# Optimization experiments

Hardware: AMD Instinct MI355X
Metric: run time of the kernel (lower is better)

The kernel has to match this reference:

```python
import jax, jax.numpy as jnp
import numpy as np
from jax import lax

B, L, D_MODEL = 2, 1024, 1024
EXPAND, D_STATE, D_CONV = 2, 16, 4
D_INNER = EXPAND * D_MODEL
DT_RANK = D_MODEL // 16  # ceil(1024/16) = 64
D_FF = 4 * D_MODEL


def setup_inputs() -> dict:
    key = jax.random.key(0)
    ks = jax.random.split(key, 20)
    s = lambda *sh: 1.0 / np.sqrt(sh[-1])
    inp = {
        "x": jax.random.normal(ks[0], (B, L, D_MODEL), jnp.float32),
        "ln1_w": jnp.ones((D_MODEL,), jnp.float32),
        "ln1_b": jnp.zeros((D_MODEL,), jnp.float32),
        "W_in": jax.random.normal(ks[1], (2 * D_INNER, D_MODEL), jnp.float32) * s(D_MODEL),
        "conv_w": jax.random.normal(ks[2], (D_INNER, D_CONV), jnp.float32) * s(D_CONV),
        "conv_b": jnp.zeros((D_INNER,), jnp.float32),
        "W_xproj": jax.random.normal(ks[3], (DT_RANK + 2 * D_STATE, D_INNER), jnp.float32) * s(D_INNER),
        "W_dt": jax.random.normal(ks[4], (D_INNER, DT_RANK), jnp.float32) * s(DT_RANK),
        "b_dt": jax.random.uniform(ks[5], (D_INNER,), jnp.float32, -4.0, -2.0),  # dt bias ~ small softplus
        "A_log": jnp.log(jnp.broadcast_to(jnp.arange(1, D_STATE + 1, dtype=jnp.float32), (D_INNER, D_STATE))),
        "D": jnp.ones((D_INNER,), jnp.float32),
        "W_out": jax.random.normal(ks[6], (D_MODEL, D_INNER), jnp.float32) * s(D_INNER),
        "ln2_w": jnp.ones((D_MODEL,), jnp.float32),
        "ln2_b": jnp.zeros((D_MODEL,), jnp.float32),
        "W1": jax.random.normal(ks[7], (D_FF, D_MODEL), jnp.float32) * s(D_MODEL),
        "b1": jnp.zeros((D_FF,), jnp.float32),
        "W2": jax.random.normal(ks[8], (D_MODEL, D_FF), jnp.float32) * s(D_FF),
        "b2": jnp.zeros((D_MODEL,), jnp.float32),
    }
    return inp


def _layernorm(x, w, b, eps=1e-5):
    mu = jnp.mean(x, axis=-1, keepdims=True)
    var = jnp.var(x, axis=-1, keepdims=True)
    return (x - mu) * lax.rsqrt(var + eps) * w + b


def _mamba(h, W_in, conv_w, conv_b, W_xproj, W_dt, b_dt, A_log, D, W_out):
    # in_proj -> [B, L, 2*d_inner]
    xz = jnp.einsum("bld,ed->ble", h, W_in)
    u, z = xz[..., :D_INNER], xz[..., D_INNER:]
    # causal depthwise conv over time
    uc = jnp.transpose(u, (0, 2, 1))  # [B, d_inner, L]
    uc = lax.conv_general_dilated(
        uc, conv_w[:, None, :], window_strides=(1,), padding=[(D_CONV - 1, 0)],
        dimension_numbers=("NCH", "OIH", "NCH"), feature_group_count=D_INNER)
    uc = jax.nn.silu(uc + conv_b[None, :, None])
    u = jnp.transpose(uc, (0, 2, 1))  # [B, L, d_inner]
    # input-dependent dt, B, C
    x_db = jnp.einsum("bld,ed->ble", u, W_xproj)
    dt = jax.nn.softplus(jnp.einsum("blr,dr->bld", x_db[..., :DT_RANK], W_dt) + b_dt)
    Bm = x_db[..., DT_RANK:DT_RANK + D_STATE]  # [B, L, d_state]
    Cm = x_db[..., DT_RANK + D_STATE:]         # [B, L, d_state]
    A = -jnp.exp(A_log)                        # [d_inner, d_state]

    def step(hst, t):
        dt_t, B_t, C_t, u_t = t  # [B,d_inner], [B,ds], [B,ds], [B,d_inner]
        dA = jnp.exp(dt_t[:, :, None] * A)                       # [B,d_inner,d_state]
        hst = dA * hst + dt_t[:, :, None] * B_t[:, None, :] * u_t[:, :, None]
        y_t = jnp.einsum("bds,bs->bd", hst, C_t)
        return hst, y_t

    h0 = jnp.zeros((u.shape[0], D_INNER, D_STATE), u.dtype)
    xs = (jnp.swapaxes(dt, 0, 1), jnp.swapaxes(Bm, 0, 1), jnp.swapaxes(Cm, 0, 1), jnp.swapaxes(u, 0, 1))
    _, ys = lax.scan(step, h0, xs)
    y = jnp.swapaxes(ys, 0, 1) + u * D  # skip term D*u
    y = y * jax.nn.silu(z)
    return jnp.einsum("ble,de->bld", y, W_out)


def reference(x, ln1_w, ln1_b, W_in, conv_w, conv_b, W_xproj, W_dt, b_dt, A_log, D,
              W_out, ln2_w, ln2_b, W1, b1, W2, b2):
    x = x + _mamba(_layernorm(x, ln1_w, ln1_b), W_in, conv_w, conv_b, W_xproj, W_dt, b_dt, A_log, D, W_out)
    h = _layernorm(x, ln2_w, ln2_b)
    ffn = jnp.einsum("blf,df->bld", jax.nn.relu(jnp.einsum("bld,fd->blf", h, W1) + b1), W2) + b2
    return x + ffn
```

## Files before the change

kernel.cpp:

```cpp
#include <hip/hip_runtime.h>

typedef unsigned short u16;
typedef unsigned int   u32;
typedef short   bf16x8 __attribute__((ext_vector_type(8)));
typedef float   f32x4  __attribute__((ext_vector_type(4)));
typedef u16     u16x4  __attribute__((ext_vector_type(4)));

__device__ __forceinline__ u16 f2b(float f) {
    u32 u = __builtin_bit_cast(u32, f);
    u32 r = u + 0x7FFFu + ((u >> 16) & 1u);
    return (u16)(r >> 16);
}
__device__ __forceinline__ float b2f(u16 h) {
    u32 u = ((u32)h) << 16;
    return __builtin_bit_cast(float, u);
}
__device__ __forceinline__ u16x4 f4_to_b4(float4 v) {
    u16x4 o; o.x = f2b(v.x); o.y = f2b(v.y); o.z = f2b(v.z); o.w = f2b(v.w);
    return o;
}

__device__ __forceinline__ float fexp2(float x) {
    float r;
    asm("v_exp_f32 %0, %1" : "=v"(r) : "v"(x));
    return r;
}
__device__ __forceinline__ float flog2(float x) {
    float r;
    asm("v_log_f32 %0, %1" : "=v"(r) : "v"(x));
    return r;
}

template <int CTRL>
__device__ __forceinline__ float dpp_add(float p) {
    int pi = __builtin_bit_cast(int, p);
    int q  = __builtin_amdgcn_update_dpp(pi, pi, CTRL, 0xF, 0xF, false);
    return p + __builtin_bit_cast(float, q);
}
#define DPP_XOR1 0xB1
#define DPP_XOR2 0x4E
#define DPP_HMIR 0x141
#define DPP_MIR  0x140

#define MROWS   2048
#define NSEG    16
#define SEGT    64
#define L2E     1.44269504088896340736f
#define LN2     0.69314718055994530942f

#define GLDS(g, l) __builtin_amdgcn_global_load_lds(                      \
    (const __attribute__((address_space(1))) void*)(g),                   \
    (__attribute__((address_space(3))) void*)(l), 16, 0, 0)

__global__ __launch_bounds__(256) void cvt_all(const float* __restrict__ W_in,
                                               const float* __restrict__ W_out,
                                               const float* __restrict__ W1,
                                               const float* __restrict__ W2,
                                               const float* __restrict__ W_dt,
                                               u16* __restrict__ Winb,
                                               u16* __restrict__ Woutb,
                                               u16* __restrict__ W1b,
                                               u16* __restrict__ W2b,
                                               u16* __restrict__ Wdtb) {
    const int i = blockIdx.x * 256 + threadIdx.x;
    const float* src; u16* dst; int off;
    if (i < 1048576)      { src = W_in;  dst = Winb;  off = i; }
    else if (i < 1572864) { src = W_out; dst = Woutb; off = i - 1048576; }
    else if (i < 2621440) { src = W1;    dst = W1b;   off = i - 1572864; }
    else if (i < 3670016) { src = W2;    dst = W2b;   off = i - 2621440; }
    else                  { src = W_dt;  dst = Wdtb;  off = i - 3670016; }
    float4 v = ((const float4*)src)[off];
    ((u16x4*)dst)[off] = f4_to_b4(v);
}

__global__ __launch_bounds__(256) void pad_xproj_kernel(const float* __restrict__ in,
                                                        u16* __restrict__ out) {
    int i = blockIdx.x * 256 + threadIdx.x;
    int r = i >> 9, c4 = i & 511;
    float4 v = make_float4(0.f, 0.f, 0.f, 0.f);
    if (r < 96) v = ((const float4*)(in + (size_t)r * 2048))[c4];
    ((u16x4*)(out + (size_t)r * 2048))[c4] = f4_to_b4(v);
}

__global__ __launch_bounds__(256) void ln_kernel(const float* __restrict__ x,
                                                 const float* __restrict__ w,
                                                 const float* __restrict__ b,
                                                 u16* __restrict__ out) {
    const int row = blockIdx.x;
    const int tid = threadIdx.x;
    const float4 v = ((const float4*)(x + (size_t)row * 1024))[tid];
    float s = v.x + v.y + v.z + v.w;
    float q = v.x * v.x + v.y * v.y + v.z * v.z + v.w * v.w;
#pragma unroll
    for (int off = 1; off < 64; off <<= 1) {
        s += __shfl_xor(s, off, 64);
        q += __shfl_xor(q, off, 64);
    }
    __shared__ float ss[4], qq[4];
    const int wave = tid >> 6;
    if ((tid & 63) == 0) { ss[wave] = s; qq[wave] = q; }
    __syncthreads();
    s = ss[0] + ss[1] + ss[2] + ss[3];
    q = qq[0] + qq[1] + qq[2] + qq[3];
    const float mean = s * (1.f / 1024.f);
    const float var  = q * (1.f / 1024.f) - mean * mean;
    const float rstd = rsqrtf(var + 1e-5f);
    const float4 wv = ((const float4*)w)[tid];
    const float4 bv = ((const float4*)b)[tid];
    float4 o;
    o.x = (v.x - mean) * rstd * wv.x + bv.x;
    o.y = (v.y - mean) * rstd * wv.y + bv.y;
    o.z = (v.z - mean) * rstd * wv.z + bv.z;
    o.w = (v.w - mean) * rstd * wv.w + bv.w;
    ((u16x4*)(out + (size_t)row * 1024))[tid] = f4_to_b4(o);
}

__global__ __launch_bounds__(256) void conv_kernel(const u16* __restrict__ xzu,
                                                   const float* __restrict__ cw,
                                                   const float* __restrict__ cb,
                                                   u16* __restrict__ utl) {
    const int idx = blockIdx.x * 256 + threadIdx.x;
    const int row = idx >> 9;
    const int d4  = idx & 511;
    const int d   = d4 * 4;
    const int bb  = row >> 10;
    const int t   = row & 1023;
    float w0[4], w1[4], w2[4], w3[4];
    *(float4*)w0 = ((const float4*)cw)[d + 0];
    *(float4*)w1 = ((const float4*)cw)[d + 1];
    *(float4*)w2 = ((const float4*)cw)[d + 2];
    *(float4*)w3 = ((const float4*)cw)[d + 3];
    float4 a = ((const float4*)cb)[d4];
#pragma unroll
    for (int j = 0; j < 4; ++j) {
        const int tt = t - 3 + j;
        if (tt >= 0) {
            const u16x4 uv = *(const u16x4*)(xzu + ((size_t)(bb * 1024 + tt)) * 2048 + d);
            a.x += b2f(uv.x) * w0[j];
            a.y += b2f(uv.y) * w1[j];
            a.z += b2f(uv.z) * w2[j];
            a.w += b2f(uv.w) * w3[j];
        }
    }
    float4 o;
    o.x = a.x / (1.f + __expf(-a.x));
    o.y = a.y / (1.f + __expf(-a.y));
    o.z = a.z / (1.f + __expf(-a.z));
    o.w = a.w / (1.f + __expf(-a.w));
    *(u16x4*)(utl + (((size_t)(d >> 4)) * 2048 + row) * 16 + (d & 15)) = f4_to_b4(o);
}

template <int EPI>
__global__ __launch_bounds__(512) void gemm_tb(const u16* __restrict__ A,
                                               const u16* __restrict__ Bw,
                                               void* __restrict__ Cptr,
                                               void* __restrict__ Cptr2,
                                               const float* __restrict__ bias,
                                               int M, int N, int K, int KS) {
    const int nbm = gridDim.x, nbn = gridDim.y;
    const int nwg = nbm * nbn;
    const int id  = blockIdx.x + nbm * blockIdx.y;
    const int sw  = (nwg >= 8) ? ((id & 7) * (nwg >> 3) + (id >> 3)) : id;
    const int bm  = sw % nbm, bn = sw / nbm;

    __shared__ u16 Asm[4][128 * 32];
    __shared__ u16 Bsm[4][128 * 32];
    const int tid  = threadIdx.x;
    const int kz   = blockIdx.z;
    const int lane = tid & 63;
    const int wave = tid >> 6;
    const int wm   = wave >> 1, wn = wave & 1;
    const u16* Ag = A  + (size_t)bm * 128 * K;
    const u16* Bg = Bw + (size_t)bn * 128 * K;
    const int r0 = tid >> 2;
    const int sg = (tid & 3) * 8;
    const int k0 = kz * KS;
    const int nk = KS >> 5;
    const int fr = lane & 15, fk = (lane >> 4) * 8;

#define STG(bf, kk)                                                            \
    {                                                                          \
        const int kof = k0 + (kk) * 32;                                        \
        GLDS(Ag + (size_t)r0 * K + kof + sg, &Asm[bf][tid * 8]);               \
        GLDS(Bg + (size_t)r0 * K + kof + sg, &Bsm[bf][tid * 8]);               \
    }

    f32x4 acc[2][4] = {};
    STG(0, 0); STG(1, 1); STG(2, 2);
    int buf = 0;
    for (int k = 0; k < nk; ++k) {
        if (k < nk - 2)       asm volatile("s_waitcnt vmcnt(4)" ::: "memory");
        else if (k == nk - 2) asm volatile("s_waitcnt vmcnt(2)" ::: "memory");
        else                  asm volatile("s_waitcnt vmcnt(0)" ::: "memory");
        __builtin_amdgcn_s_barrier();
        bf16x8 a[2], b[4];
#pragma unroll
        for (int m = 0; m < 2; ++m)
            a[m] = *(const bf16x8*)&Asm[buf][(wm * 32 + m * 16 + fr) * 32 + fk];
#pragma unroll
        for (int n = 0; n < 4; ++n)
            b[n] = *(const bf16x8*)&Bsm[buf][(wn * 64 + n * 16 + fr) * 32 + fk];
        if (k + 3 < nk) STG((buf + 3) & 3, k + 3);
#pragma unroll
        for (int m = 0; m < 2; ++m)
#pragma unroll
            for (int n = 0; n < 4; ++n)
                acc[m][n] = __builtin_amdgcn_mfma_f32_16x16x32_bf16(a[m], b[n], acc[m][n], 0, 0, 0);
        buf = (buf + 1) & 3;
    }
#undef STG

    const int fq = lane >> 4;
#pragma unroll
    for (int m = 0; m < 2; ++m) {
#pragma unroll
        for (int n = 0; n < 4; ++n) {
            const int row0 = bm * 128 + wm * 32 + m * 16 + fq * 4;
            const int col  = bn * 128 + wn * 64 + n * 16 + fr;
#pragma unroll
            for (int j = 0; j < 4; ++j) {
                float v = acc[m][n][j];
                if constexpr (EPI == 3) {
                    v += bias[col];
                    ((u16*)Cptr)[(size_t)(row0 + j) * N + col] = f2b(fmaxf(v, 0.f));
                } else if constexpr (EPI == 5) {
                    if (col < 2048) {
                        ((u16*)Cptr)[(size_t)(row0 + j) * 2048 + col] = f2b(v);
                    } else {
                        const float sv = v / (1.f + __expf(-v));
                        const int zc = col - 2048;
                        ((u16*)Cptr2)[(((size_t)(zc >> 4)) * 2048 + row0 + j) * 16 + (zc & 15)]
                            = f2b(sv);
                    }
                } else {
                    ((float*)Cptr)[(size_t)kz * M * N + (size_t)(row0 + j) * N + col] = v;
                }
            }
        }
    }
}

__global__ __launch_bounds__(256) void gemm_xp(const u16* __restrict__ utl,
                                               const u16* __restrict__ Bw,
                                               float* __restrict__ part) {
    const int nwg = 16;
    const int id  = blockIdx.x;
    const int sw  = (id & 7) * (nwg >> 3) + (id >> 3);
    const int bm  = sw;
    __shared__ u16 Asm[4][128 * 32];
    __shared__ u16 Bsm[4][128 * 32];
    const int tid  = threadIdx.x;
    const int kz   = blockIdx.z;
    const int lane = tid & 63;
    const int wave = tid >> 6;
    const int wm   = wave >> 1, wn = wave & 1;
    const u16* Bg = Bw;
    const int r0 = tid >> 2;
    const int pc = tid & 3;
    const int sg = pc * 8;
    const int k0 = kz * 256;
    const int fr = lane & 15, fk = (lane >> 4) * 8;

#define STGX(bf, kk)                                                                     \
    {                                                                                    \
        const int kof = k0 + (kk) * 32;                                                  \
        const int kc  = kof >> 4;                                                        \
        GLDS(utl + ((size_t)(kc + (pc >> 1)) * 2048 + bm * 128 + r0) * 16 + (pc & 1) * 8,\
             &Asm[bf][tid * 8]);                                                         \
        GLDS(utl + ((size_t)(kc + (pc >> 1)) * 2048 + bm * 128 + r0 + 64) * 16 + (pc & 1) * 8,\
             &Asm[bf][(tid + 256) * 8]);                                                 \
        GLDS(Bg + (size_t)r0 * 2048 + kof + sg, &Bsm[bf][tid * 8]);                      \
        GLDS(Bg + (size_t)(r0 + 64) * 2048 + kof + sg, &Bsm[bf][(tid + 256) * 8]);       \
    }

    f32x4 acc[4][4] = {};
    STGX(0, 0); STGX(1, 1); STGX(2, 2);
    int buf = 0;
    const int nk = 8;
    for (int k = 0; k < nk; ++k) {
        if (k < nk - 2)       asm volatile("s_waitcnt vmcnt(8)" ::: "memory");
        else if (k == nk - 2) asm volatile("s_waitcnt vmcnt(4)" ::: "memory");
        else                  asm volatile("s_waitcnt vmcnt(0)" ::: "memory");
        __builtin_amdgcn_s_barrier();
        bf16x8 a[4], b[4];
#pragma unroll
        for (int m = 0; m < 4; ++m)
            a[m] = *(const bf16x8*)&Asm[buf][(wm * 64 + m * 16 + fr) * 32 + fk];
#pragma unroll
        for (int n = 0; n < 4; ++n)
            b[n] = *(const bf16x8*)&Bsm[buf][(wn * 64 + n * 16 + fr) * 32 + fk];
        if (k + 3 < nk) STGX((buf + 3) & 3, k + 3);
#pragma unroll
        for (int m = 0; m < 4; ++m)
#pragma unroll
            for (int n = 0; n < 4; ++n)
                acc[m][n] = __builtin_amdgcn_mfma_f32_16x16x32_bf16(a[m], b[n], acc[m][n], 0, 0, 0);
        buf = (buf + 1) & 3;
    }
#undef STGX

    const int fq = lane >> 4;
    float* Cp = part + (size_t)kz * MROWS * 128;
#pragma unroll
    for (int m = 0; m < 4; ++m) {
#pragma unroll
        for (int n = 0; n < 4; ++n) {
            const int row0 = bm * 128 + wm * 64 + m * 16 + fq * 4;
            const int col  = wn * 64 + n * 16 + fr;
#pragma unroll
            for (int j = 0; j < 4; ++j)
                Cp[(size_t)(row0 + j) * 128 + col] = acc[m][n][j];
        }
    }
}

__global__ __launch_bounds__(256) void xproj_combine(const float* __restrict__ part,
                                                     u16* __restrict__ xdbr,
                                                     float* __restrict__ bcp) {
    int i = blockIdx.x * 256 + threadIdx.x;
    int row = i >> 5, c4 = i & 31;
    if (c4 >= 24) return;
    float4 s = make_float4(0.f, 0.f, 0.f, 0.f);
#pragma unroll
    for (int p = 0; p < 8; ++p) {
        float4 v = ((const float4*)(part + (size_t)p * MROWS * 128 + (size_t)row * 128))[c4];
        s.x += v.x; s.y += v.y; s.z += v.z; s.w += v.w;
    }
    if (c4 < 16) {
        ((u16x4*)(xdbr + (size_t)row * 64))[c4] = f4_to_b4(s);
    } else {
        const int e0 = (c4 - 16) * 4;
        float sv[4] = {s.x, s.y, s.z, s.w};
#pragma unroll
        for (int j = 0; j < 4; ++j) {
            const int e = e0 + j;
            const int st  = (e < 16) ? e : (e - 16);
            const int isc = (e < 16) ? 0 : 1;
            bcp[(size_t)(row >> 1) * 64 + st * 4 + (row & 1) * 2 + isc] = sv[j];
        }
    }
}

__device__ __forceinline__ void compute_dtu_tile(const u16* __restrict__ xdbr,
                                                 const u16* __restrict__ Wdtb,
                                                 const float* __restrict__ b_dt,
                                                 const u16* __restrict__ utile,
                                                 float* __restrict__ du_s,
                                                 size_t t0, int d0, int w, int l) {
    const int fr = l & 15, fk = (l >> 4) * 8;
    const bf16x8 a0 = *(const bf16x8*)(xdbr + (t0 + w * 16 + fr) * 64 + fk);
    const bf16x8 a1 = *(const bf16x8*)(xdbr + (t0 + w * 16 + fr) * 64 + 32 + fk);
    const bf16x8 b0 = *(const bf16x8*)(Wdtb + (size_t)(d0 + fr) * 64 + fk);
    const bf16x8 b1 = *(const bf16x8*)(Wdtb + (size_t)(d0 + fr) * 64 + 32 + fk);
    const float bdt = b_dt[d0 + fr];
    f32x4 acc = {};
    acc = __builtin_amdgcn_mfma_f32_16x16x32_bf16(a0, b0, acc, 0, 0, 0);
    acc = __builtin_amdgcn_mfma_f32_16x16x32_bf16(a1, b1, acc, 0, 0, 0);
#pragma unroll
    for (int j = 0; j < 4; ++j) {
        const int row = w * 16 + (l >> 4) * 4 + j;
        float v = acc[j] + bdt;
        const float sp = flog2(1.f + fexp2(v * L2E)) * LN2;
        v = (v > 20.f) ? v : sp;
        const float uval = b2f(utile[(t0 + row) * 16 + fr]);
        float2 dv; dv.x = v; dv.y = v * uval;
        *(float2*)&du_s[(row >> 1) * 66 + fr * 4 + (row & 1) * 2] = dv;
    }
}

__device__ __forceinline__ void stage_bc(const float* __restrict__ bcp,
                                         float* __restrict__ bc_s,
                                         size_t p0, int w, int l) {
    const int pr = (w << 3) + (l >> 4);
    const int pc = (l & 15) << 2;
    GLDS(bcp + (p0 + pr) * 64 + pc,     &bc_s[(w << 9)]);
    GLDS(bcp + (p0 + pr + 4) * 64 + pc, &bc_s[(w << 9) + 256]);
}

__global__ __launch_bounds__(256) void scan_pass1(const u16* __restrict__ xdbr,
                                                  const u16* __restrict__ Wdtb,
                                                  const float* __restrict__ b_dt,
                                                  const u16* __restrict__ utl,
                                                  const float* __restrict__ bcp,
                                                  const float* __restrict__ A_log,
                                                  float* __restrict__ Qarr,
                                                  float* __restrict__ Sarr) {
    __shared__ __align__(16) float du_s[32 * 66];
    __shared__ __align__(16) float bc_s[32 * 64];

    const int tid = threadIdx.x;
    const int l   = tid & 63;
    const int w   = tid >> 6;
    const int s   = l & 15;
    const int g   = (w << 2) | (l >> 4);
    const int d0  = blockIdx.x << 4;
    const int b   = blockIdx.y;
    const int seg = blockIdx.z;
    const int d   = d0 + g;
    const size_t t0 = (size_t)b * 1024 + (size_t)seg * SEGT;
    const u16* utile = utl + (size_t)(d0 >> 4) * 2048 * 16;

    stage_bc(bcp, bc_s, t0 >> 1, w, l);
    compute_dtu_tile(xdbr, Wdtb, b_dt, utile, du_s, t0, d0, w, l);

    const float As2 = -__expf(A_log[d * 16 + s]) * L2E;
    asm volatile("s_waitcnt vmcnt(0) lgkmcnt(0)" ::: "memory");
    __builtin_amdgcn_s_barrier();

    float Q = 0.f, S = 0.f;
#pragma unroll 8
    for (int t2 = 0; t2 < 32; ++t2) {
        const float4 du4 = *(const float4*)&du_s[t2 * 66 + g * 4];
        const float4 BC2 = *(const float4*)&bc_s[t2 * 64 + s * 4];
        S += du4.x;
        Q = fexp2(du4.x * As2) * Q + du4.y * BC2.x;
        S += du4.z;
        Q = fexp2(du4.z * As2) * Q + du4.w * BC2.z;
    }
    Qarr[(((size_t)seg * 2 + b) * 2048 + d) * 16 + s] = Q;
    if (s == 0) Sarr[((size_t)seg * 2 + b) * 2048 + d] = S;
}

__global__ __launch_bounds__(256) void scan_prefix(const float* __restrict__ Qarr,
                                                   const float* __restrict__ Sarr,
                                                   const float* __restrict__ A_log,
                                                   float* __restrict__ H0) {
    const int tid = threadIdx.x;
    const int d   = (blockIdx.x << 4) + (tid >> 4);
    const int s   = tid & 15;
    const int b   = blockIdx.y;
    const float As2 = -__expf(A_log[d * 16 + s]) * L2E;
    float h = 0.f;
#pragma unroll
    for (int i = 0; i < NSEG; ++i) {
        const size_t base = ((size_t)i * 2 + b) * 2048 + d;
        H0[base * 16 + s] = h;
        h = fexp2(As2 * Sarr[base]) * h + Qarr[base * 16 + s];
    }
}

__global__ __launch_bounds__(256) void scan_pass2(const u16* __restrict__ xdbr,
                                                  const u16* __restrict__ Wdtb,
                                                  const float* __restrict__ b_dt,
                                                  const u16* __restrict__ utl,
                                                  const float* __restrict__ bcp,
                                                  const u16* __restrict__ zst,
                                                  const float* __restrict__ A_log,
                                                  const float* __restrict__ Dp,
                                                  const float* __restrict__ H0,
                                                  u16* __restrict__ ymul) {
    __shared__ __align__(16) float du_s[32 * 66];
    __shared__ __align__(16) float bc_s[32 * 64];

    const int tid = threadIdx.x;
    const int l   = tid & 63;
    const int w   = tid >> 6;
    const int s   = l & 15;
    const int g   = (w << 2) | (l >> 4);
    const int d0  = blockIdx.x << 4;
    const int b   = blockIdx.y;
    const int seg = blockIdx.z;
    const int d   = d0 + g;
    const size_t t0 = (size_t)b * 1024 + (size_t)seg * SEGT;
    const u16* utile = utl + (size_t)(d0 >> 4) * 2048 * 16;
    const u16* ztile = zst + (size_t)(d0 >> 4) * 2048 * 16;

    stage_bc(bcp, bc_s, t0 >> 1, w, l);
    compute_dtu_tile(xdbr, Wdtb, b_dt, utile, du_s, t0, d0, w, l);

    const float As2 = -__expf(A_log[d * 16 + s]) * L2E;
    float h = H0[(((size_t)seg * 2 + b) * 2048 + d) * 16 + s];

    asm volatile("s_waitcnt vmcnt(0) lgkmcnt(0)" ::: "memory");
    __builtin_amdgcn_s_barrier();

    float pk[4];
#pragma unroll
    for (int c = 0; c < 4; ++c) {
        pk[c] = 0.f;
#pragma unroll
        for (int q = 0; q < 8; ++q) {
            const int t2 = c * 8 + q;
            const float4 du4 = *(const float4*)&du_s[t2 * 66 + g * 4];
            const float4 BC2 = *(const float4*)&bc_s[t2 * 64 + s * 4];
            h = fexp2(du4.x * As2) * h + du4.y * BC2.x;
            float p = h * BC2.y;
            p = dpp_add<DPP_XOR1>(p);
            p = dpp_add<DPP_XOR2>(p);
            p = dpp_add<DPP_HMIR>(p);
            p = dpp_add<DPP_MIR>(p);
            {
                const unsigned long long km = 0x0001000100010001ULL << (2 * q);
                asm("v_cndmask_b32 %0, %0, %1, %2" : "+v"(pk[c]) : "v"(p), "s"(km));
            }
            h = fexp2(du4.z * As2) * h + du4.w * BC2.z;
            p = h * BC2.w;
            p = dpp_add<DPP_XOR1>(p);
            p = dpp_add<DPP_XOR2>(p);
            p = dpp_add<DPP_HMIR>(p);
            p = dpp_add<DPP_MIR>(p);
            {
                const unsigned long long km = 0x0001000100010001ULL << (2 * q + 1);
                asm("v_cndmask_b32 %0, %0, %1, %2" : "+v"(pk[c]) : "v"(p), "s"(km));
            }
        }
    }

    __builtin_amdgcn_s_barrier();
    float* p_s = du_s;
#pragma unroll
    for (int c = 0; c < 4; ++c) {
        const int row = c * 16 + s;
        p_s[row * 16 + (g ^ (row & 12))] = pk[c];
    }

    asm volatile("s_waitcnt lgkmcnt(0)" ::: "memory");
    __builtin_amdgcn_s_barrier();

    {
        const int tt = tid >> 2, cc = (tid & 3) << 2;
        const float4 pv = *(const float4*)&p_s[tt * 16 + (cc ^ (tt & 12))];
        const u16x4  uv = *(const u16x4*)(utile + (t0 + tt) * 16 + cc);
        const u16x4  zs = *(const u16x4*)(ztile + (t0 + tt) * 16 + cc);
        const float4 Dv = *(const float4*)(Dp + d0 + cc);
        float4 o;
        o.x = (pv.x + b2f(uv.x) * Dv.x) * b2f(zs.x);
        o.y = (pv.y + b2f(uv.y) * Dv.y) * b2f(zs.y);
        o.z = (pv.z + b2f(uv.z) * Dv.z) * b2f(zs.z);
        o.w = (pv.w + b2f(uv.w) * Dv.w) * b2f(zs.w);
        *(u16x4*)(ymul + (t0 + tt) * 2048 + d0 + cc) = f4_to_b4(o);
    }
}

__global__ __launch_bounds__(256) void ffn2_combine(const float* __restrict__ part,
                                                    const float* __restrict__ x2,
                                                    const float* __restrict__ b2,
                                                    float* __restrict__ out) {
    int i = blockIdx.x * 256 + threadIdx.x;
    float4 s = ((const float4*)x2)[i];
    float4 bv = ((const float4*)b2)[i & 255];
    s.x += bv.x; s.y += bv.y; s.z += bv.z; s.w += bv.w;
#pragma unroll
    for (int p = 0; p < 4; ++p) {
        float4 v = ((const float4*)(part + (size_t)p * MROWS * 1024))[i];
        s.x += v.x; s.y += v.y; s.z += v.z; s.w += v.w;
    }
    ((float4*)out)[i] = s;
}

__global__ __launch_bounds__(256) void outproj_combine_ln2(const float* __restrict__ x,
                                                           const float* __restrict__ part,
                                                           const float* __restrict__ w,
                                                           const float* __restrict__ b,
                                                           float* __restrict__ x2,
                                                           u16* __restrict__ h2) {
    const int row = blockIdx.x;
    const int tid = threadIdx.x;
    float4 v = ((const float4*)(x + (size_t)row * 1024))[tid];
    float4 p0 = ((const float4*)(part + (size_t)row * 1024))[tid];
    float4 p1 = ((const float4*)(part + (size_t)MROWS * 1024 + (size_t)row * 1024))[tid];
    v.x += p0.x + p1.x; v.y += p0.y + p1.y; v.z += p0.z + p1.z; v.w += p0.w + p1.w;
    ((float4*)(x2 + (size_t)row * 1024))[tid] = v;
    float s = v.x + v.y + v.z + v.w;
    float q = v.x * v.x + v.y * v.y + v.z * v.z + v.w * v.w;
#pragma unroll
    for (int off = 1; off < 64; off <<= 1) {
        s += __shfl_xor(s, off, 64);
        q += __shfl_xor(q, off, 64);
    }
    __shared__ float ss[4], qq[4];
    const int wave = tid >> 6;
    if ((tid & 63) == 0) { ss[wave] = s; qq[wave] = q; }
    __syncthreads();
    s = ss[0] + ss[1] + ss[2] + ss[3];
    q = qq[0] + qq[1] + qq[2] + qq[3];
    const float mean = s * (1.f / 1024.f);
    const float var  = q * (1.f / 1024.f) - mean * mean;
    const float rstd = rsqrtf(var + 1e-5f);
    const float4 wv = ((const float4*)w)[tid];
    const float4 bv = ((const float4*)b)[tid];
    float4 o;
    o.x = (v.x - mean) * rstd * wv.x + bv.x;
    o.y = (v.y - mean) * rstd * wv.y + bv.y;
    o.z = (v.z - mean) * rstd * wv.z + bv.z;
    o.w = (v.w - mean) * rstd * wv.w + bv.w;
    ((u16x4*)(h2 + (size_t)row * 1024))[tid] = f4_to_b4(o);
}

extern "C" void kernel_launch(void* const* d_in, const int* in_sizes, int n_in,
                              void* d_out, int out_size, void* d_ws, size_t ws_size,
                              hipStream_t stream) {
    const float* x      = (const float*)d_in[0];
    const float* ln1_w  = (const float*)d_in[1];
    const float* ln1_b  = (const float*)d_in[2];
    const float* W_in   = (const float*)d_in[3];
    const float* conv_w = (const float*)d_in[4];
    const float* conv_b = (const float*)d_in[5];
    const float* W_xproj= (const float*)d_in[6];
    const float* W_dt   = (const float*)d_in[7];
    const float* b_dt   = (const float*)d_in[8];
    const float* A_log  = (const float*)d_in[9];
    const float* Dvec   = (const float*)d_in[10];
    const float* W_out  = (const float*)d_in[11];
    const float* ln2_w  = (const float*)d_in[12];
    const float* ln2_b  = (const float*)d_in[13];
    const float* W1     = (const float*)d_in[14];
    const float* b1     = (const float*)d_in[15];
    const float* W2     = (const float*)d_in[16];
    const float* b2     = (const float*)d_in[17];
    float* out = (float*)d_out;
    char*  ws  = (char*)d_ws;
    const size_t MB = 1024ull * 1024ull;

    u16*   h1b   = (u16*)(ws + 0);
    u16*   xzu   = (u16*)(ws + 4 * MB);
    u16*   zst   = (u16*)(ws + 12 * MB);
    u16*   utl   = (u16*)(ws + 20 * MB);
    float* parts = (float*)(ws + 28 * MB);
    float* bcp   = (float*)(ws + 36 * MB);
    u16*   xdbr  = (u16*)(ws + 36 * MB + 256 * 1024);
    u16*   Wdtb  = (u16*)(ws + 36 * MB + 512 * 1024);
    u16*   ymul  = (u16*)(ws + 37 * MB);
    float* Qarr  = (float*)(ws + 45 * MB);
    float* Sarr  = (float*)(ws + 49 * MB);
    float* H0    = (float*)(ws + 50 * MB);
    float* x2    = (float*)(ws + 54 * MB);
    u16*   Winb  = (u16*)(ws + 62 * MB);
    u16*   Woutb = (u16*)(ws + 70 * MB);
    u16*   W1b   = (u16*)(ws + 74 * MB);
    u16*   W2b   = (u16*)(ws + 82 * MB);
    u16*   Wxpb  = (u16*)(ws + 90 * MB);
    u16*   h2b   = h1b;
    float* opart = (float*)(ws + 4 * MB);
    u16*   f1    = (u16*)(ws + 4 * MB);
    float* fpart = (float*)(ws + 20 * MB);

    cvt_all<<<14464, 256, 0, stream>>>(W_in, W_out, W1, W2, W_dt,
                                       Winb, Woutb, W1b, W2b, Wdtb);
    pad_xproj_kernel<<<256, 256, 0, stream>>>(W_xproj, Wxpb);

    ln_kernel<<<2048, 256, 0, stream>>>(x, ln1_w, ln1_b, h1b);
    gemm_tb<5><<<dim3(16, 32, 1), 512, 0, stream>>>(h1b, Winb, xzu, zst, nullptr,
                                                    MROWS, 4096, 1024, 1024);
    conv_kernel<<<4096, 256, 0, stream>>>(xzu, conv_w, conv_b, utl);
    gemm_xp<<<dim3(16, 1, 8), 256, 0, stream>>>(utl, Wxpb, parts);
    xproj_combine<<<256, 256, 0, stream>>>(parts, xdbr, bcp);
    scan_pass1<<<dim3(128, 2, NSEG), 256, 0, stream>>>(xdbr, Wdtb, b_dt, utl, bcp, A_log,
                                                       Qarr, Sarr);
    scan_prefix<<<dim3(128, 2), 256, 0, stream>>>(Qarr, Sarr, A_log, H0);
    scan_pass2<<<dim3(128, 2, NSEG), 256, 0, stream>>>(xdbr, Wdtb, b_dt, utl, bcp, zst,
                                                       A_log, Dvec, H0, ymul);
    gemm_tb<10><<<dim3(16, 8, 2), 512, 0, stream>>>(ymul, Woutb, opart, nullptr, nullptr,
                                                    MROWS, 1024, 2048, 1024);
    outproj_combine_ln2<<<2048, 256, 0, stream>>>(x, opart, ln2_w, ln2_b, x2, h2b);
    gemm_tb<3><<<dim3(16, 32, 1), 512, 0, stream>>>(h2b, W1b, f1, nullptr, b1,
                                                    MROWS, 4096, 1024, 1024);
    gemm_tb<10><<<dim3(16, 8, 4), 512, 0, stream>>>(f1, W2b, fpart, nullptr, nullptr,
                                                    MROWS, 1024, 4096, 1024);
    ffn2_combine<<<2048, 256, 0, stream>>>(fpart, x2, b2, out);
}
```

Before: 217.0 us.

## Shrink GEMM LDS ring to three stages and pack B-only buffer for scan pass1

Both GEMM kernels move from a 4-slot, 3-ahead shared-memory prefetch ring to a 3-slot, 2-ahead ring, with adjusted vmcnt waits. This cuts LDS use per block, which can raise occupancy, at the cost of less latency hiding. Separately, xproj_combine now also writes a packed B-only array so scan_pass1 can stage half as much data into LDS with a single direct global-to-LDS load, instead of staging the interleaved B/C buffer.

```diff
diff --git a/kernel.cpp b/kernel.cpp
--- a/kernel.cpp
+++ b/kernel.cpp
@@ -163,8 +163,8 @@
     const int sw  = (nwg >= 8) ? ((id & 7) * (nwg >> 3) + (id >> 3)) : id;
     const int bm  = sw % nbm, bn = sw / nbm;
 
-    __shared__ u16 Asm[4][128 * 32];
-    __shared__ u16 Bsm[4][128 * 32];
+    __shared__ u16 Asm[3][128 * 32];
+    __shared__ u16 Bsm[3][128 * 32];
     const int tid  = threadIdx.x;
     const int kz   = blockIdx.z;
     const int lane = tid & 63;
@@ -186,12 +186,11 @@
     }
 
     f32x4 acc[2][4] = {};
-    STG(0, 0); STG(1, 1); STG(2, 2);
+    STG(0, 0); STG(1, 1);
     int buf = 0;
     for (int k = 0; k < nk; ++k) {
-        if (k < nk - 2)       asm volatile("s_waitcnt vmcnt(4)" ::: "memory");
-        else if (k == nk - 2) asm volatile("s_waitcnt vmcnt(2)" ::: "memory");
-        else                  asm volatile("s_waitcnt vmcnt(0)" ::: "memory");
+        if (k < nk - 1) asm volatile("s_waitcnt vmcnt(2)" ::: "memory");
+        else            asm volatile("s_waitcnt vmcnt(0)" ::: "memory");
         __builtin_amdgcn_s_barrier();
         bf16x8 a[2], b[4];
 #pragma unroll
@@ -200,13 +199,16 @@
 #pragma unroll
         for (int n = 0; n < 4; ++n)
             b[n] = *(const bf16x8*)&Bsm[buf][(wn * 64 + n * 16 + fr) * 32 + fk];
-        if (k + 3 < nk) STG((buf + 3) & 3, k + 3);
+        if (k + 2 < nk) {
+            const int slot = (buf + 2) % 3;
+            STG(slot, k + 2);
+        }
 #pragma unroll
         for (int m = 0; m < 2; ++m)
 #pragma unroll
             for (int n = 0; n < 4; ++n)
                 acc[m][n] = __builtin_amdgcn_mfma_f32_16x16x32_bf16(a[m], b[n], acc[m][n], 0, 0, 0);
-        buf = (buf + 1) & 3;
+        buf = (buf == 2) ? 0 : buf + 1;
     }
 #undef STG
 
@@ -247,8 +249,8 @@
     const int id  = blockIdx.x;
     const int sw  = (id & 7) * (nwg >> 3) + (id >> 3);
     const int bm  = sw;
-    __shared__ u16 Asm[4][128 * 32];
-    __shared__ u16 Bsm[4][128 * 32];
+    __shared__ u16 Asm[3][128 * 32];
+    __shared__ u16 Bsm[3][128 * 32];
     const int tid  = threadIdx.x;
     const int kz   = blockIdx.z;
     const int lane = tid & 63;
@@ -274,13 +276,12 @@
     }
 
     f32x4 acc[4][4] = {};
-    STGX(0, 0); STGX(1, 1); STGX(2, 2);
+    STGX(0, 0); STGX(1, 1);
     int buf = 0;
     const int nk = 8;
     for (int k = 0; k < nk; ++k) {
-        if (k < nk - 2)       asm volatile("s_waitcnt vmcnt(8)" ::: "memory");
-        else if (k == nk - 2) asm volatile("s_waitcnt vmcnt(4)" ::: "memory");
-        else                  asm volatile("s_waitcnt vmcnt(0)" ::: "memory");
+        if (k < nk - 1) asm volatile("s_waitcnt vmcnt(4)" ::: "memory");
+        else            asm volatile("s_waitcnt vmcnt(0)" ::: "memory");
         __builtin_amdgcn_s_barrier();
         bf16x8 a[4], b[4];
 #pragma unroll
@@ -289,13 +290,16 @@
 #pragma unroll
         for (int n = 0; n < 4; ++n)
             b[n] = *(const bf16x8*)&Bsm[buf][(wn * 64 + n * 16 + fr) * 32 + fk];
-        if (k + 3 < nk) STGX((buf + 3) & 3, k + 3);
+        if (k + 2 < nk) {
+            const int slot = (buf + 2) % 3;
+            STGX(slot, k + 2);
+        }
 #pragma unroll
         for (int m = 0; m < 4; ++m)
 #pragma unroll
             for (int n = 0; n < 4; ++n)
                 acc[m][n] = __builtin_amdgcn_mfma_f32_16x16x32_bf16(a[m], b[n], acc[m][n], 0, 0, 0);
-        buf = (buf + 1) & 3;
+        buf = (buf == 2) ? 0 : buf + 1;
     }
 #undef STGX
 
@@ -316,7 +320,8 @@
 
 __global__ __launch_bounds__(256) void xproj_combine(const float* __restrict__ part,
                                                      u16* __restrict__ xdbr,
-                                                     float* __restrict__ bcp) {
+                                                     float* __restrict__ bcp,
+                                                     float* __restrict__ bpk) {
     int i = blockIdx.x * 256 + threadIdx.x;
     int row = i >> 5, c4 = i & 31;
     if (c4 >= 24) return;
@@ -337,6 +342,8 @@
             const int st  = (e < 16) ? e : (e - 16);
             const int isc = (e < 16) ? 0 : 1;
             bcp[(size_t)(row >> 1) * 64 + st * 4 + (row & 1) * 2 + isc] = sv[j];
+            if (e < 16)
+                bpk[(size_t)(row >> 1) * 32 + st * 2 + (row & 1)] = sv[j];
         }
     }
 }
@@ -381,12 +388,12 @@
                                                   const u16* __restrict__ Wdtb,
                                                   const float* __restrict__ b_dt,
                                                   const u16* __restrict__ utl,
-                                                  const float* __restrict__ bcp,
+                                                  const float* __restrict__ bpk,
                                                   const float* __restrict__ A_log,
                                                   float* __restrict__ Qarr,
                                                   float* __restrict__ Sarr) {
     __shared__ __align__(16) float du_s[32 * 66];
-    __shared__ __align__(16) float bc_s[32 * 64];
+    __shared__ __align__(16) float bp_s[32 * 32];
 
     const int tid = threadIdx.x;
     const int l   = tid & 63;
@@ -400,7 +407,7 @@
     const size_t t0 = (size_t)b * 1024 + (size_t)seg * SEGT;
     const u16* utile = utl + (size_t)(d0 >> 4) * 2048 * 16;
 
-    stage_bc(bcp, bc_s, t0 >> 1, w, l);
+    GLDS(bpk + ((t0 >> 1) + (tid >> 3)) * 32 + ((tid & 7) << 2), &bp_s[w << 8]);
     compute_dtu_tile(xdbr, Wdtb, b_dt, utile, du_s, t0, d0, w, l);
 
     const float As2 = -__expf(A_log[d * 16 + s]) * L2E;
@@ -411,11 +418,11 @@
 #pragma unroll 8
     for (int t2 = 0; t2 < 32; ++t2) {
         const float4 du4 = *(const float4*)&du_s[t2 * 66 + g * 4];
-        const float4 BC2 = *(const float4*)&bc_s[t2 * 64 + s * 4];
+        const float2 Bp  = *(const float2*)&bp_s[t2 * 32 + s * 2];
         S += du4.x;
-        Q = fexp2(du4.x * As2) * Q + du4.y * BC2.x;
+        Q = fexp2(du4.x * As2) * Q + du4.y * Bp.x;
         S += du4.z;
-        Q = fexp2(du4.z * As2) * Q + du4.w * BC2.z;
+        Q = fexp2(du4.z * As2) * Q + du4.w * Bp.y;
     }
     Qarr[(((size_t)seg * 2 + b) * 2048 + d) * 16 + s] = Q;
     if (s == 0) Sarr[((size_t)seg * 2 + b) * 2048 + d] = S;
@@ -620,6 +627,7 @@
     float* bcp   = (float*)(ws + 36 * MB);
     u16*   xdbr  = (u16*)(ws + 36 * MB + 256 * 1024);
     u16*   Wdtb  = (u16*)(ws + 36 * MB + 512 * 1024);
+    float* bpk   = (float*)(ws + 36 * MB + 768 * 1024);
     u16*   ymul  = (u16*)(ws + 37 * MB);
     float* Qarr  = (float*)(ws + 45 * MB);
     float* Sarr  = (float*)(ws + 49 * MB);
@@ -644,8 +652,8 @@
                                                     MROWS, 4096, 1024, 1024);
     conv_kernel<<<4096, 256, 0, stream>>>(xzu, conv_w, conv_b, utl);
     gemm_xp<<<dim3(16, 1, 8), 256, 0, stream>>>(utl, Wxpb, parts);
-    xproj_combine<<<256, 256, 0, stream>>>(parts, xdbr, bcp);
-    scan_pass1<<<dim3(128, 2, NSEG), 256, 0, stream>>>(xdbr, Wdtb, b_dt, utl, bcp, A_log,
+    xproj_combine<<<256, 256, 0, stream>>>(parts, xdbr, bcp, bpk);
+    scan_pass1<<<dim3(128, 2, NSEG), 256, 0, stream>>>(xdbr, Wdtb, b_dt, utl, bpk, A_log,
                                                        Qarr, Sarr);
     scan_prefix<<<dim3(128, 2), 256, 0, stream>>>(Qarr, Sarr, A_log, H0);
     scan_pass2<<<dim3(128, 2, NSEG), 256, 0, stream>>>(xdbr, Wdtb, b_dt, utl, bcp, zst,
```

Measured after the change: 216.2 us. Within noise of the previous version (-0.4%).
